# Optimization experiments

Hardware: AMD Instinct MI355X
Metric: run time of the kernel (lower is better)

The kernel has to match this reference:

```python
import jax, jax.numpy as jnp
import numpy as np

EPS = 1e-6          # epsilon for ray-triangle intersection
HIT_TOL = 1e-3      # hit tolerance for occlusion test (t < 1 - HIT_TOL)
MIN_LEN = 1.2e-6    # ~10 * float32 eps, minimal squared segment length


def _dot(u, v=None, keepdims=False):
    v = u if v is None else v
    return jnp.sum(u * v, axis=-1, keepdims=keepdims)


def _rays_intersect_triangles(ro, rd, tv):
    # Moller-Trumbore. ro/rd: [..., 3]; tv: [..., 3, 3] (broadcastable).
    v0 = tv[..., 0, :]
    e1 = tv[..., 1, :] - v0
    e2 = tv[..., 2, :] - v0
    h = jnp.cross(rd, e2)
    a = _dot(e1, h)
    cond_a = jnp.abs(a) < EPS
    f = jnp.where(cond_a, 0.0, 1.0 / jnp.where(cond_a, 1.0, a))
    s = ro - v0
    u = f * _dot(s, h)
    q = jnp.cross(s, e1)
    v = f * _dot(rd, q)
    t = f * _dot(e2, q)
    hit = (~cond_a) & (u >= 0.0) & (u <= 1.0) & (v >= 0.0) & (u + v <= 1.0) & (t > EPS)
    return t, hit


def _image_method(tx_b, rx_b, mirror_vertices, mirror_normals):
    # tx_b/rx_b: [T,R,P,3]; mirror_vertices/normals: [P,order,3]
    mv = jnp.moveaxis(mirror_vertices, 1, 0)  # [order,P,3]
    mn = jnp.moveaxis(mirror_normals, 1, 0)

    def fwd(carry, x):
        m_v, m_n = x
        img = carry - 2.0 * _dot(carry - m_v, m_n, keepdims=True) * m_n
        return img, img

    _, images = jax.lax.scan(fwd, tx_b, (mv, mn))

    def bwd(carry, x):
        m_v, m_n, img = x
        u = carry - img
        un = _dot(u, m_n, keepdims=True)
        vn = _dot(img - m_v, m_n, keepdims=True)
        bad = un == 0.0
        t = jnp.where(bad, 0.0, -vn / jnp.where(bad, 1.0, un))
        p = img + t * u
        return p, p

    _, paths = jax.lax.scan(bwd, rx_b, (mv, mn, images), reverse=True)
    return jnp.moveaxis(paths, 0, -2)  # [T,R,P,order,3]


def _forward(mesh_vertices, mesh_triangles, tx_vertices, rx_vertices, path_candidates):
    T, R = tx_vertices.shape[0], rx_vertices.shape[0]
    P, order = path_candidates.shape
    tv_all = mesh_vertices[mesh_triangles]  # [NF,3,3]
    fn = jnp.cross(tv_all[:, 1] - tv_all[:, 0], tv_all[:, 2] - tv_all[:, 0])
    normals = fn / jnp.linalg.norm(fn, axis=-1, keepdims=True)  # [NF,3]
    tri_v = tv_all[path_candidates]          # [P,order,3,3]
    mirror_vertices = tri_v[..., 0, :]       # [P,order,3]
    mirror_normals = normals[path_candidates]
    tx_b = jnp.broadcast_to(tx_vertices[:, None, None, :], (T, R, P, 3))
    rx_b = jnp.broadcast_to(rx_vertices[None, :, None, :], (T, R, P, 3))
    paths = _image_method(tx_b, rx_b, mirror_vertices, mirror_normals)
    full_paths = jnp.concatenate((tx_b[..., None, :], paths, rx_b[..., None, :]), axis=-2)  # [T,R,P,order+2,3]
    ro = full_paths[..., :-1, :]
    rd = jnp.diff(full_paths, axis=-2)
    # reflection points lie inside their triangles
    _, hit_in = _rays_intersect_triangles(ro[..., :-1, :], rd[..., :-1, :], tri_v)
    inside = hit_in.all(axis=-1)
    # consecutive vertices on same side of each mirror
    d_prev = _dot(full_paths[..., :-2, :] - mirror_vertices, mirror_normals)
    d_next = _dot(full_paths[..., 2:, :] - mirror_vertices, mirror_normals)
    valid_refl = (d_prev * d_next >= 0.0).all(axis=-1)
    # occlusion: any segment blocked by any triangle
    t_all, hit_all = _rays_intersect_triangles(ro[..., None, :], rd[..., None, :], tv_all)
    blocked = (hit_all & (t_all < 1.0 - HIT_TOL)).any(axis=-1).any(axis=-1)
    too_small = (_dot(rd) < MIN_LEN).any(axis=-1)
    mask = inside & valid_refl & (~blocked) & (~too_small)
    return full_paths, mask


def setup_inputs():
    key = jax.random.key(0)
    k1, k2, k3, k4, k5 = jax.random.split(key, 5)
    NV, NF, T, R, P, ORDER = 3000, 600, 2, 4, 1000, 2
    return {
        "mesh_vertices": jax.random.normal(k1, (NV, 3), dtype=jnp.float32),
        "mesh_triangles": jax.random.randint(k2, (NF, 3), 0, NV, dtype=jnp.int32),
        "tx_vertices": jax.random.normal(k3, (T, 3), dtype=jnp.float32),
        "rx_vertices": jax.random.normal(k4, (R, 3), dtype=jnp.float32),
        "path_candidates": jax.random.randint(k5, (P, ORDER), 0, NF, dtype=jnp.int32),
    }


def reference(mesh_vertices, mesh_triangles, tx_vertices, rx_vertices, path_candidates):
    full_paths, mask = _forward(mesh_vertices, mesh_triangles, tx_vertices, rx_vertices, path_candidates)
    T, R = tx_vertices.shape[0], rx_vertices.shape[0]
    P, order = path_candidates.shape
    dt = path_candidates.dtype
    tx_obj = jnp.broadcast_to(jnp.arange(T, dtype=dt)[:, None, None, None], (T, R, P, 1))
    rx_obj = jnp.broadcast_to(jnp.arange(R, dtype=dt)[None, :, None, None], (T, R, P, 1))
    pc = jnp.broadcast_to(path_candidates, (T, R, P, order))
    objects = jnp.concatenate((tx_obj, pc, rx_obj), axis=-1)
    return full_paths, objects, mask
```

## Files before the change

kernel.cpp:

```cpp
#include <hip/hip_runtime.h>


#define DEV __device__ __forceinline__

struct F3 { float x, y, z; };

DEV float fmul(float a, float b) { return __fmul_rn(a, b); }
DEV float fadd(float a, float b) { return __fadd_rn(a, b); }
DEV float fsub(float a, float b) { return __fsub_rn(a, b); }

DEV F3 f3sub(F3 a, F3 b) { return { fsub(a.x,b.x), fsub(a.y,b.y), fsub(a.z,b.z) }; }
DEV float f3dot(F3 a, F3 b) {
  return fadd(fadd(fmul(a.x,b.x), fmul(a.y,b.y)), fmul(a.z,b.z));
}
DEV F3 f3cross(F3 a, F3 b) {
  return { fsub(fmul(a.y,b.z), fmul(a.z,b.y)),
           fsub(fmul(a.z,b.x), fmul(a.x,b.z)),
           fsub(fmul(a.x,b.y), fmul(a.y,b.x)) };
}

struct MTRes { float t; bool hit; };

DEV MTRes mt(F3 ro, F3 rd, F3 v0, F3 e1, F3 e2) {
  F3 h = f3cross(rd, e2);
  float a = f3dot(e1, h);
  bool conda = fabsf(a) < 1e-6f;
  float f = conda ? 0.0f : __fdiv_rn(1.0f, a);
  F3 s = f3sub(ro, v0);
  float u = fmul(f, f3dot(s, h));
  F3 q = f3cross(s, e1);
  float v = fmul(f, f3dot(rd, q));
  float tt = fmul(f, f3dot(e2, q));
  bool hit = (!conda) && (u >= 0.0f) && (u <= 1.0f) && (v >= 0.0f)
             && (fadd(u, v) <= 1.0f) && (tt > 1e-6f);
  return { tt, hit };
}

__global__ void k_pretri(const float* __restrict__ verts, const int* __restrict__ tris,
                         float4* __restrict__ out, int nf) {
  int f = blockIdx.x * blockDim.x + threadIdx.x;
  if (f >= nf) return;
  int i0 = tris[3*f+0], i1 = tris[3*f+1], i2 = tris[3*f+2];
  F3 v0 = { verts[3*i0], verts[3*i0+1], verts[3*i0+2] };
  F3 v1 = { verts[3*i1], verts[3*i1+1], verts[3*i1+2] };
  F3 v2 = { verts[3*i2], verts[3*i2+1], verts[3*i2+2] };
  F3 e1 = f3sub(v1, v0);
  F3 e2 = f3sub(v2, v0);
  F3 fn = f3cross(e1, e2);
  float nrm = __fsqrt_rn(fadd(fadd(fmul(fn.x,fn.x), fmul(fn.y,fn.y)), fmul(fn.z,fn.z)));
  F3 n = { __fdiv_rn(fn.x, nrm), __fdiv_rn(fn.y, nrm), __fdiv_rn(fn.z, nrm) };
  out[3*f+0] = make_float4(v0.x, v0.y, v0.z, e1.x);
  out[3*f+1] = make_float4(e1.y, e1.z, e2.x, e2.y);
  out[3*f+2] = make_float4(e2.z, n.x, n.y, n.z);
}

__global__ __launch_bounds__(256) void k_paths(
    const float* __restrict__ txv, const float* __restrict__ rxv,
    const int* __restrict__ pc, const float4* __restrict__ tri,
    float* __restrict__ out, int T, int R, int P, int nf)
{
  const int lane = threadIdx.x & 63;
  const int pw = blockIdx.x * 4 + (threadIdx.x >> 6);
  const int nPaths = T * R * P;
  if (pw >= nPaths) return;
  const int p  = pw % P;
  const int tr = pw / P;
  const int r  = tr % R;
  const int t  = tr / R;

  const int f0 = pc[2*p + 0];
  const int f1 = pc[2*p + 1];
  float4 a0 = tri[3*f0], b0 = tri[3*f0+1], c0 = tri[3*f0+2];
  float4 a1 = tri[3*f1], b1 = tri[3*f1+1], c1 = tri[3*f1+2];
  F3 v00 = {a0.x,a0.y,a0.z}, e10 = {a0.w,b0.x,b0.y}, e20 = {b0.z,b0.w,c0.x}, n0 = {c0.y,c0.z,c0.w};
  F3 v01 = {a1.x,a1.y,a1.z}, e11 = {a1.w,b1.x,b1.y}, e21 = {b1.z,b1.w,c1.x}, n1 = {c1.y,c1.z,c1.w};

  F3 TX = { txv[3*t], txv[3*t+1], txv[3*t+2] };
  F3 RX = { rxv[3*r], rxv[3*r+1], rxv[3*r+2] };

  float d0  = f3dot(f3sub(TX, v00), n0);
  float td0 = fmul(2.0f, d0);
  F3 img1 = { fsub(TX.x, fmul(td0, n0.x)), fsub(TX.y, fmul(td0, n0.y)), fsub(TX.z, fmul(td0, n0.z)) };
  float d1  = f3dot(f3sub(img1, v01), n1);
  float td1 = fmul(2.0f, d1);
  F3 img2 = { fsub(img1.x, fmul(td1, n1.x)), fsub(img1.y, fmul(td1, n1.y)), fsub(img1.z, fmul(td1, n1.z)) };

  F3 u2 = f3sub(RX, img2);
  float un = f3dot(u2, n1);
  float vn = f3dot(f3sub(img2, v01), n1);
  float tb = (un == 0.0f) ? 0.0f : __fdiv_rn(-vn, un);
  F3 p1 = { fadd(img2.x, fmul(tb, u2.x)), fadd(img2.y, fmul(tb, u2.y)), fadd(img2.z, fmul(tb, u2.z)) };

  F3 u1 = f3sub(p1, img1);
  un = f3dot(u1, n0);
  vn = f3dot(f3sub(img1, v00), n0);
  tb = (un == 0.0f) ? 0.0f : __fdiv_rn(-vn, un);
  F3 p0 = { fadd(img1.x, fmul(tb, u1.x)), fadd(img1.y, fmul(tb, u1.y)), fadd(img1.z, fmul(tb, u1.z)) };

  F3 ro0 = TX, ro1 = p0, ro2 = p1;
  F3 rd0 = f3sub(p0, TX), rd1 = f3sub(p1, p0), rd2 = f3sub(RX, p1);

  MTRes h0 = mt(ro0, rd0, v00, e10, e20);
  MTRes h1 = mt(ro1, rd1, v01, e11, e21);
  bool inside = h0.hit && h1.hit;

  float dp0 = f3dot(f3sub(TX, v00), n0);
  float dn0 = f3dot(f3sub(p1, v00), n0);
  float dp1 = f3dot(f3sub(p0, v01), n1);
  float dn1 = f3dot(f3sub(RX, v01), n1);
  bool vrefl = (fmul(dp0, dn0) >= 0.0f) && (fmul(dp1, dn1) >= 0.0f);

  bool toosmall = (f3dot(rd0, rd0) < 1.2e-6f) ||
                  (f3dot(rd1, rd1) < 1.2e-6f) ||
                  (f3dot(rd2, rd2) < 1.2e-6f);

  bool pre = inside && vrefl && !toosmall;
  bool blocked = false;
  if (pre) {
    bool blk = false;
    for (int f = lane; f < nf; f += 64) {
      float4 aa = tri[3*f], bb = tri[3*f+1], cc = tri[3*f+2];
      F3 w0  = {aa.x, aa.y, aa.z};
      F3 we1 = {aa.w, bb.x, bb.y};
      F3 we2 = {bb.z, bb.w, cc.x};
      MTRes hb0 = mt(ro0, rd0, w0, we1, we2);
      MTRes hb1 = mt(ro1, rd1, w0, we1, we2);
      MTRes hb2 = mt(ro2, rd2, w0, we1, we2);
      blk = blk || (hb0.hit && (hb0.t < 0.999f))
                || (hb1.hit && (hb1.t < 0.999f))
                || (hb2.hit && (hb2.t < 0.999f));
    }
    blocked = (__ballot(blk) != 0ULL);
  }
  bool mask = pre && !blocked;

  if (lane == 0) {
    float4* fp = reinterpret_cast<float4*>(out) + (size_t)pw * 3;
    fp[0] = make_float4(TX.x, TX.y, TX.z, p0.x);
    fp[1] = make_float4(p0.y, p0.z, p1.x, p1.y);
    fp[2] = make_float4(p1.z, RX.x, RX.y, RX.z);
    float4* ob = reinterpret_cast<float4*>(out + (size_t)nPaths * 12) + pw;
    *ob = make_float4((float)t, (float)f0, (float)f1, (float)r);
    out[(size_t)nPaths * 16 + pw] = mask ? 1.0f : 0.0f;
  }
}

extern "C" void kernel_launch(void* const* d_in, const int* in_sizes, int n_in,
                              void* d_out, int out_size, void* d_ws, size_t ws_size,
                              hipStream_t stream) {
  const float* mesh_v = (const float*)d_in[0];
  const int*   mesh_t = (const int*)d_in[1];
  const float* txv    = (const float*)d_in[2];
  const float* rxv    = (const float*)d_in[3];
  const int*   pc     = (const int*)d_in[4];

  const int NF = in_sizes[1] / 3;
  const int T  = in_sizes[2] / 3;
  const int R  = in_sizes[3] / 3;
  const int P  = in_sizes[4] / 2;

  float4* tris = (float4*)d_ws;

  k_pretri<<<(NF + 255) / 256, 256, 0, stream>>>(mesh_v, mesh_t, tris, NF);

  const int nPaths = T * R * P;
  const int blocks = (nPaths + 3) / 4;
  k_paths<<<blocks, 256, 0, stream>>>(txv, rxv, pc, tris, (float*)d_out,
                                      T, R, P, NF);
}
```

Baseline: 77.04 us.

## Fuse triangle precompute into path kernel and stage triangles in shared memory

Removes the separate triangle-precompute kernel. Each block now recomputes every triangle's vertex, edges and normal into LDS, using a stride-13 layout to avoid bank conflicts, and then reads triangle data from LDS during the path and occlusion passes. This drops one launch and the global-memory round trip. In exchange, all 2000 blocks redo the full 600-triangle precompute with gathers and divisions/sqrt, and about 31 KB of LDS per block may limit occupancy.

```diff
diff --git a/kernel.cpp b/kernel.cpp
--- a/kernel.cpp
+++ b/kernel.cpp
@@ -36,29 +36,35 @@
   return { tt, hit };
 }
 
-__global__ void k_pretri(const float* __restrict__ verts, const int* __restrict__ tris,
-                         float4* __restrict__ out, int nf) {
-  int f = blockIdx.x * blockDim.x + threadIdx.x;
-  if (f >= nf) return;
-  int i0 = tris[3*f+0], i1 = tris[3*f+1], i2 = tris[3*f+2];
-  F3 v0 = { verts[3*i0], verts[3*i0+1], verts[3*i0+2] };
-  F3 v1 = { verts[3*i1], verts[3*i1+1], verts[3*i1+2] };
-  F3 v2 = { verts[3*i2], verts[3*i2+1], verts[3*i2+2] };
-  F3 e1 = f3sub(v1, v0);
-  F3 e2 = f3sub(v2, v0);
-  F3 fn = f3cross(e1, e2);
-  float nrm = __fsqrt_rn(fadd(fadd(fmul(fn.x,fn.x), fmul(fn.y,fn.y)), fmul(fn.z,fn.z)));
-  F3 n = { __fdiv_rn(fn.x, nrm), __fdiv_rn(fn.y, nrm), __fdiv_rn(fn.z, nrm) };
-  out[3*f+0] = make_float4(v0.x, v0.y, v0.z, e1.x);
-  out[3*f+1] = make_float4(e1.y, e1.z, e2.x, e2.y);
-  out[3*f+2] = make_float4(e2.z, n.x, n.y, n.z);
-}
+#define FSTRIDE 13
 
-__global__ __launch_bounds__(256) void k_paths(
+__global__ __launch_bounds__(256) void k_fused(
+    const float* __restrict__ verts, const int* __restrict__ trisIdx,
     const float* __restrict__ txv, const float* __restrict__ rxv,
-    const int* __restrict__ pc, const float4* __restrict__ tri,
-    float* __restrict__ out, int T, int R, int P, int nf)
+    const int* __restrict__ pc, float* __restrict__ out,
+    int T, int R, int P, int nf)
 {
+  extern __shared__ float sf[];
+
+  for (int f = threadIdx.x; f < nf; f += blockDim.x) {
+    int i0 = trisIdx[3*f+0], i1 = trisIdx[3*f+1], i2 = trisIdx[3*f+2];
+    F3 v0 = { verts[3*i0], verts[3*i0+1], verts[3*i0+2] };
+    F3 v1 = { verts[3*i1], verts[3*i1+1], verts[3*i1+2] };
+    F3 v2 = { verts[3*i2], verts[3*i2+1], verts[3*i2+2] };
+    F3 e1 = f3sub(v1, v0);
+    F3 e2 = f3sub(v2, v0);
+    F3 fn = f3cross(e1, e2);
+    float nrm = __fsqrt_rn(fadd(fadd(fmul(fn.x,fn.x), fmul(fn.y,fn.y)), fmul(fn.z,fn.z)));
+    float* s = sf + (size_t)f * FSTRIDE;
+    s[0] = v0.x; s[1] = v0.y; s[2] = v0.z;
+    s[3] = e1.x; s[4] = e1.y; s[5] = e1.z;
+    s[6] = e2.x; s[7] = e2.y; s[8] = e2.z;
+    s[9]  = __fdiv_rn(fn.x, nrm);
+    s[10] = __fdiv_rn(fn.y, nrm);
+    s[11] = __fdiv_rn(fn.z, nrm);
+  }
+  __syncthreads();
+
   const int lane = threadIdx.x & 63;
   const int pw = blockIdx.x * 4 + (threadIdx.x >> 6);
   const int nPaths = T * R * P;
@@ -70,10 +76,10 @@
 
   const int f0 = pc[2*p + 0];
   const int f1 = pc[2*p + 1];
-  float4 a0 = tri[3*f0], b0 = tri[3*f0+1], c0 = tri[3*f0+2];
-  float4 a1 = tri[3*f1], b1 = tri[3*f1+1], c1 = tri[3*f1+2];
-  F3 v00 = {a0.x,a0.y,a0.z}, e10 = {a0.w,b0.x,b0.y}, e20 = {b0.z,b0.w,c0.x}, n0 = {c0.y,c0.z,c0.w};
-  F3 v01 = {a1.x,a1.y,a1.z}, e11 = {a1.w,b1.x,b1.y}, e21 = {b1.z,b1.w,c1.x}, n1 = {c1.y,c1.z,c1.w};
+  const float* s0 = sf + (size_t)f0 * FSTRIDE;
+  const float* s1 = sf + (size_t)f1 * FSTRIDE;
+  F3 v00 = {s0[0],s0[1],s0[2]}, e10 = {s0[3],s0[4],s0[5]}, e20 = {s0[6],s0[7],s0[8]}, n0 = {s0[9],s0[10],s0[11]};
+  F3 v01 = {s1[0],s1[1],s1[2]}, e11 = {s1[3],s1[4],s1[5]}, e21 = {s1[6],s1[7],s1[8]}, n1 = {s1[9],s1[10],s1[11]};
 
   F3 TX = { txv[3*t], txv[3*t+1], txv[3*t+2] };
   F3 RX = { rxv[3*r], rxv[3*r+1], rxv[3*r+2] };
@@ -119,10 +125,10 @@
   if (pre) {
     bool blk = false;
     for (int f = lane; f < nf; f += 64) {
-      float4 aa = tri[3*f], bb = tri[3*f+1], cc = tri[3*f+2];
-      F3 w0  = {aa.x, aa.y, aa.z};
-      F3 we1 = {aa.w, bb.x, bb.y};
-      F3 we2 = {bb.z, bb.w, cc.x};
+      const float* s = sf + (size_t)f * FSTRIDE;
+      F3 w0  = {s[0], s[1], s[2]};
+      F3 we1 = {s[3], s[4], s[5]};
+      F3 we2 = {s[6], s[7], s[8]};
       MTRes hb0 = mt(ro0, rd0, w0, we1, we2);
       MTRes hb1 = mt(ro1, rd1, w0, we1, we2);
       MTRes hb2 = mt(ro2, rd2, w0, we1, we2);
@@ -159,12 +165,10 @@
   const int R  = in_sizes[3] / 3;
   const int P  = in_sizes[4] / 2;
 
-  float4* tris = (float4*)d_ws;
-
-  k_pretri<<<(NF + 255) / 256, 256, 0, stream>>>(mesh_v, mesh_t, tris, NF);
-
   const int nPaths = T * R * P;
   const int blocks = (nPaths + 3) / 4;
-  k_paths<<<blocks, 256, 0, stream>>>(txv, rxv, pc, tris, (float*)d_out,
-                                      T, R, P, NF);
+  const size_t shmem = (size_t)NF * FSTRIDE * sizeof(float);
+
+  k_fused<<<blocks, 256, shmem, stream>>>(mesh_v, mesh_t, txv, rxv, pc,
+                                          (float*)d_out, T, R, P, NF);
 }
```

Result: no change. 77.95 us (+1.2%).
